# Performance work log

Hardware: AMD Instinct MI355X
Metric: run time of the kernel (lower is better)

## Reference

```python
import jax, jax.numpy as jnp
import numpy as np

NUM_NET = 2
V = 100000
D = 128
B = 4096
K = 5
NS = 10
HYP1 = 0.1
HYP2 = 0.1
HYP3 = 0.1


def setup_inputs() -> dict:
    key = jax.random.key(0)
    ks = jax.random.split(key, 10)
    ri = lambda k, shape: jax.random.randint(k, shape, 0, V, dtype=jnp.int32)
    return {
        "node_tables": jax.random.normal(ks[0], (NUM_NET, V, D), jnp.float32) * 0.1,
        "neigh_tables": jax.random.normal(ks[1], (NUM_NET, V, D), jnp.float32) * 0.1,
        "nodes_idx": ri(ks[2], (NUM_NET, B)),
        "neigh_idx": ri(ks[3], (NUM_NET, B, K)),
        "role_idx": ri(ks[4], (NUM_NET, NUM_NET, B)),
        "neg_main": ri(ks[5], (NUM_NET, B, K * NS)),
        "neg_node": ri(ks[6], (NUM_NET, NUM_NET, B, 1 * NS)),
        "neg_cross": ri(ks[7], (NUM_NET, NUM_NET, B, K * NS)),
        "neg_role": ri(ks[8], (NUM_NET, NUM_NET, B, 1 * NS)),
    }


def _pos_loss(ctx, node):
    # ctx: (B, M, D), node: (B, D) -> mean over all logsigmoid(ctx . node)
    return jax.nn.log_sigmoid(jnp.einsum("bmd,bd->bm", ctx, node)).mean()


def _neg_loss(neg_ctx, node):
    # ctx embeddings are negated: logsigmoid(-(neg . node)), sum over samples, mean over batch
    return jax.nn.log_sigmoid(-jnp.einsum("bmd,bd->bm", neg_ctx, node)).sum(axis=1).mean()


def reference(node_tables, neigh_tables, nodes_idx, neigh_idx, role_idx,
              neg_main, neg_node, neg_cross, neg_role):
    cost = []
    for i in range(NUM_NET):
        node_emb = node_tables[i][nodes_idx[i]]          # (B, D)
        # main SGNS loss on view i (neigh tables)
        neigh_emb = neigh_tables[i][neigh_idx[i]]        # (B, K, D)
        c = _pos_loss(neigh_emb, node_emb) + _neg_loss(neigh_tables[i][neg_main[i]], node_emb)
        cost.append(c)
        # cross-view node alignment (node tables of j at same node indices)
        for j in range(NUM_NET):
            if j != i:
                ctx = node_tables[j][nodes_idx[i]][:, None, :]   # (B, 1, D)
                c = _pos_loss(ctx, node_emb) + _neg_loss(node_tables[j][neg_node[i, j]], node_emb)
                cost.append(HYP1 * c)
        # cross-view neighbor loss (neigh tables of j at view-i neighbor indices)
        for j in range(NUM_NET):
            if j != i:
                ctx = neigh_tables[j][neigh_idx[i]]              # (B, K, D)
                c = _pos_loss(ctx, node_emb) + _neg_loss(neigh_tables[j][neg_cross[i, j]], node_emb)
                cost.append(HYP2 * c)
        # role-based loss (node tables of all j at role indices)
        for j in range(NUM_NET):
            ctx = node_tables[j][role_idx[i, j]][:, None, :]     # (B, 1, D)
            c = _pos_loss(ctx, node_emb) + _neg_loss(node_tables[j][neg_role[i, j]], node_emb)
            cost.append(HYP3 * c)
    total = cost[0]
    for c in cost[1:]:
        total = total + c
    return -total / len(cost)
```

## Files before the change

kernel.cpp:

```cpp
#include <hip/hip_runtime.h>

#define NUM_NET 2
#define V 100000
#define D 128
#define B 4096
#define K 5
#define NS 10

#define W_A (1.0f/20480.0f)
#define W_B (1.0f/4096.0f)
#define W_C (0.1f/4096.0f)
#define W_D (0.1f/20480.0f)

#define NBINS 64
#define PIPE 4

template <int CTRL>
__device__ __forceinline__ float dpp_xadd(float v) {
    int r = __builtin_amdgcn_update_dpp(0, __float_as_int(v), CTRL, 0xF, 0xF, true);
    return v + __int_as_float(r);
}

__device__ __forceinline__ float lsig(float x) {
    return fminf(x, 0.0f) - __logf(1.0f + __expf(-fabsf(x)));
}

__global__ __launch_bounds__(256) void rmne_main(
    const float* __restrict__ node_tables,
    const float* __restrict__ neigh_tables,
    const int*   __restrict__ nodes_idx,
    const int*   __restrict__ neigh_idx,
    const int*   __restrict__ role_idx,
    const int*   __restrict__ neg_main,
    const int*   __restrict__ neg_node,
    const int*   __restrict__ neg_cross,
    const int*   __restrict__ neg_role,
    float*       __restrict__ ws)
{
    const int tid  = threadIdx.x;
    const int lane = tid & 63;
    const int wave = tid >> 6;
    const int unit = blockIdx.x * 4 + wave;
    const int i = unit >> 12;
    const int b = unit & (B - 1);
    const int j = 1 - i;

    int pk[3];
    #pragma unroll
    for (int s = 0; s < 3; ++s) {
        int d = lane + 64 * s;
        int idx = 0; int tab = 0;
        if      (d <   5) { idx = neigh_idx[(i*B + b)*K + d];             tab = 2 + i; }
        else if (d <  55) { idx = neg_main[(i*B + b)*50 + (d-5)];         tab = 2 + i; }
        else if (d <  56) { idx = nodes_idx[i*B + b];                     tab = j;     }
        else if (d <  66) { idx = neg_node[((i*2+j)*B + b)*NS + (d-56)];  tab = j;     }
        else if (d <  71) { idx = neigh_idx[(i*B + b)*K + (d-66)];        tab = 2 + j; }
        else if (d < 121) { idx = neg_cross[((i*2+j)*B + b)*50 + (d-71)]; tab = 2 + j; }
        else if (d < 122) { idx = role_idx[(i*2+0)*B + b];                tab = 0;     }
        else if (d < 132) { idx = neg_role[((i*2+0)*B + b)*NS + (d-122)]; tab = 0;     }
        else if (d < 133) { idx = role_idx[(i*2+1)*B + b];                tab = 1;     }
        else if (d < 143) { idx = neg_role[((i*2+1)*B + b)*NS + (d-133)]; tab = 1;     }
        pk[s] = idx | (tab << 20);
    }

    const int l16     = lane & 15;
    const int quarter = lane >> 4;
    const int nrow    = nodes_idx[i*B + b];
    const float4* nep = (const float4*)(node_tables + ((size_t)i*V + (size_t)nrow)*D) + l16*2;
    const float4 ne0 = nep[0];
    const float4 ne1 = nep[1];

    float4 c0b[PIPE], c1b[PIPE];

    auto issue = [&](int t) {
        int s   = t >> 4;
        int src = (4*t + quarter) & 63;
        int p   = __shfl(pk[s], src, 64);
        int idx = p & 0xFFFFF;
        int tab = p >> 20;
        const float* base = (tab & 2) ? neigh_tables : node_tables;
        const float4* row = (const float4*)(base + ((size_t)(tab & 1)*V + (size_t)idx)*D) + l16*2;
        c0b[t & (PIPE-1)] = row[0];
        c1b[t & (PIPE-1)] = row[1];
    };

    float accA = 0.0f, accB = 0.0f, accC = 0.0f, accG = 0.0f;

    #pragma unroll
    for (int t = 0; t < PIPE; ++t) issue(t);

    #pragma unroll
    for (int t = 0; t < 36; ++t) {
        if (t + PIPE < 36) issue(t + PIPE);
        float4 c0 = c0b[t & (PIPE-1)];
        float4 c1 = c1b[t & (PIPE-1)];
        float pp = ne0.x*c0.x + ne0.y*c0.y + ne0.z*c0.z + ne0.w*c0.w
                 + ne1.x*c1.x + ne1.y*c1.y + ne1.z*c1.z + ne1.w*c1.w;
        pp = dpp_xadd<0xB1>(pp);
        pp = dpp_xadd<0x4E>(pp);
        pp = dpp_xadd<0x124>(pp);
        pp = dpp_xadd<0x128>(pp);

        if (t == 0) {
            accA += lsig(pp);
        } else if (t == 1) {
            float x  = (quarter == 0) ? pp : -pp;
            float mw = (quarter == 0) ? W_A : W_B;
            accG = fmaf(mw, lsig(x), accG);
        } else if (t <= 12) {
            accB += lsig(-pp);
        } else if (t == 13) {
            float x  = (quarter == 3) ? pp : -pp;
            float mw = (quarter == 3) ? W_C : W_B;
            accG = fmaf(mw, lsig(x), accG);
        } else if (t <= 15) {
            accC += lsig(-pp);
        } else if (t == 16) {
            float x  = (quarter >= 2) ? pp : -pp;
            float mw = (quarter >= 2) ? W_D : W_C;
            accG = fmaf(mw, lsig(x), accG);
        } else if (t == 17) {
            float x  = (quarter == 3) ? -pp : pp;
            float mw = (quarter == 3) ? W_C : W_D;
            accG = fmaf(mw, lsig(x), accG);
        } else if (t <= 29) {
            accC += lsig(-pp);
        } else if (t == 30) {
            float x = (quarter == 1) ? pp : -pp;
            accC += lsig(x);
        } else if (t <= 32) {
            accC += lsig(-pp);
        } else if (t == 33) {
            float x = (quarter == 0) ? pp : -pp;
            accC += lsig(x);
        } else if (t == 34) {
            accC += lsig(-pp);
        } else {
            float ls = lsig(-pp);
            accC += (quarter == 3) ? 0.0f : ls;
        }
    }

    float acc = W_A*accA + W_B*accB + W_C*accC + accG;

    acc += __shfl_xor(acc, 16, 64);
    acc += __shfl_xor(acc, 32, 64);

    __shared__ float wsum[4];
    if (lane == 0) wsum[wave] = acc;
    __syncthreads();
    if (tid == 0) {
        float s = wsum[0] + wsum[1] + wsum[2] + wsum[3];
        atomicAdd(ws + (blockIdx.x & (NBINS - 1)), s);
    }
}

__global__ void rmne_finalize(const float* __restrict__ ws, float* __restrict__ out)
{
    float v = ws[threadIdx.x];
    v += __shfl_xor(v, 1, 64);
    v += __shfl_xor(v, 2, 64);
    v += __shfl_xor(v, 4, 64);
    v += __shfl_xor(v, 8, 64);
    v += __shfl_xor(v, 16, 64);
    v += __shfl_xor(v, 32, 64);
    if (threadIdx.x == 0) out[0] = v * (-1.0f / 10.0f);
}

extern "C" void kernel_launch(void* const* d_in, const int* in_sizes, int n_in,
                              void* d_out, int out_size, void* d_ws, size_t ws_size,
                              hipStream_t stream) {
    const float* node_tables  = (const float*)d_in[0];
    const float* neigh_tables = (const float*)d_in[1];
    const int*   nodes_idx    = (const int*)d_in[2];
    const int*   neigh_idx    = (const int*)d_in[3];
    const int*   role_idx     = (const int*)d_in[4];
    const int*   neg_main     = (const int*)d_in[5];
    const int*   neg_node     = (const int*)d_in[6];
    const int*   neg_cross    = (const int*)d_in[7];
    const int*   neg_role     = (const int*)d_in[8];
    float* ws  = (float*)d_ws;
    float* out = (float*)d_out;

    hipMemsetAsync(ws, 0, NBINS * sizeof(float), stream);
    rmne_main<<<2048, 256, 0, stream>>>(node_tables, neigh_tables, nodes_idx, neigh_idx,
                                        role_idx, neg_main, neg_node, neg_cross, neg_role, ws);
    rmne_finalize<<<1, 64, 0, stream>>>(ws, out);
}
```

Measured before the change: 255.4 us.

## Hand-schedule gather loads with inline asm and explicit vmcnt waits

Row gathers now go through inline global_load_dwordx4 pairs, and each step waits only on the oldest outstanding load with an exact s_waitcnt vmcnt count, so several row fetches stay in flight. The loop is fully compile-time unrolled so the buffer slots and branch selection are constants, and each refill is issued after that step's compute. Each lane now reads two 16-byte chunks 256 bytes apart instead of 32 contiguous bytes, so 16 lanes cover a contiguous 256-byte span per instruction. Inline asm and sched barriers limit the compiler's own scheduling, and the hand-written wait counts must match the issue order exactly.

```diff
diff --git a/kernel.cpp b/kernel.cpp
--- a/kernel.cpp
+++ b/kernel.cpp
@@ -1,4 +1,5 @@
 #include <hip/hip_runtime.h>
+#include <utility>
 
 #define NUM_NET 2
 #define V 100000
@@ -13,7 +14,16 @@
 #define W_D (0.1f/20480.0f)
 
 #define NBINS 64
-#define PIPE 4
+#define DEPTH 4
+
+template <class F, int... Is>
+__device__ __forceinline__ void sfor_impl(F&& f, std::integer_sequence<int, Is...>) {
+    (f(std::integral_constant<int, Is>{}), ...);
+}
+template <int N, class F>
+__device__ __forceinline__ void sfor(F&& f) {
+    sfor_impl((F&&)f, std::make_integer_sequence<int, N>{});
+}
 
 template <int CTRL>
 __device__ __forceinline__ float dpp_xadd(float v) {
@@ -23,6 +33,20 @@
 
 __device__ __forceinline__ float lsig(float x) {
     return fminf(x, 0.0f) - __logf(1.0f + __expf(-fabsf(x)));
+}
+
+__device__ __forceinline__ void gload2(float4& d0, float4& d1, const float* addr) {
+    asm volatile("global_load_dwordx4 %0, %2, off\n\t"
+                 "global_load_dwordx4 %1, %2, off offset:256"
+                 : "=&v"(d0), "=&v"(d1)
+                 : "v"(addr)
+                 : "memory");
+}
+
+template <int N>
+__device__ __forceinline__ void waitfor() {
+    asm volatile("s_waitcnt vmcnt(%0)" :: "i"(N) : "memory");
+    __builtin_amdgcn_sched_barrier(0);
 }
 
 __global__ __launch_bounds__(256) void rmne_main(
@@ -66,34 +90,37 @@
     const int l16     = lane & 15;
     const int quarter = lane >> 4;
     const int nrow    = nodes_idx[i*B + b];
-    const float4* nep = (const float4*)(node_tables + ((size_t)i*V + (size_t)nrow)*D) + l16*2;
-    const float4 ne0 = nep[0];
-    const float4 ne1 = nep[1];
-
-    float4 c0b[PIPE], c1b[PIPE];
-
-    auto issue = [&](int t) {
-        int s   = t >> 4;
-        int src = (4*t + quarter) & 63;
-        int p   = __shfl(pk[s], src, 64);
+    const float* nep  = node_tables + ((size_t)i*V + (size_t)nrow)*D + l16*4;
+
+    float4 c0b[DEPTH], c1b[DEPTH];
+    float4 ne0, ne1;
+
+    auto issue = [&](auto tc) {
+        constexpr int T = decltype(tc)::value;
+        constexpr int S = T >> 4;
+        int src = (4*T + quarter) & 63;
+        int p   = __shfl(pk[S], src, 64);
         int idx = p & 0xFFFFF;
         int tab = p >> 20;
         const float* base = (tab & 2) ? neigh_tables : node_tables;
-        const float4* row = (const float4*)(base + ((size_t)(tab & 1)*V + (size_t)idx)*D) + l16*2;
-        c0b[t & (PIPE-1)] = row[0];
-        c1b[t & (PIPE-1)] = row[1];
+        const float* addr = base + ((size_t)(tab & 1)*V + (size_t)idx)*D + l16*4;
+        gload2(c0b[T & (DEPTH-1)], c1b[T & (DEPTH-1)], addr);
     };
 
+    asm volatile("s_waitcnt vmcnt(0)" ::: "memory");
+
+    gload2(ne0, ne1, nep);
+    sfor<DEPTH>([&](auto tc) { issue(tc); });
+
     float accA = 0.0f, accB = 0.0f, accC = 0.0f, accG = 0.0f;
 
-    #pragma unroll
-    for (int t = 0; t < PIPE; ++t) issue(t);
-
-    #pragma unroll
-    for (int t = 0; t < 36; ++t) {
-        if (t + PIPE < 36) issue(t + PIPE);
-        float4 c0 = c0b[t & (PIPE-1)];
-        float4 c1 = c1b[t & (PIPE-1)];
+    sfor<36>([&](auto tc) {
+        constexpr int T   = decltype(tc)::value;
+        constexpr int INF = (36 - T) < DEPTH ? (36 - T) : DEPTH;
+        waitfor<2*(INF-1)>();
+
+        float4 c0 = c0b[T & (DEPTH-1)];
+        float4 c1 = c1b[T & (DEPTH-1)];
         float pp = ne0.x*c0.x + ne0.y*c0.y + ne0.z*c0.z + ne0.w*c0.w
                  + ne1.x*c1.x + ne1.y*c1.y + ne1.z*c1.z + ne1.w*c1.w;
         pp = dpp_xadd<0xB1>(pp);
@@ -101,45 +128,47 @@
         pp = dpp_xadd<0x124>(pp);
         pp = dpp_xadd<0x128>(pp);
 
-        if (t == 0) {
+        if constexpr (T == 0) {
             accA += lsig(pp);
-        } else if (t == 1) {
+        } else if constexpr (T == 1) {
             float x  = (quarter == 0) ? pp : -pp;
             float mw = (quarter == 0) ? W_A : W_B;
             accG = fmaf(mw, lsig(x), accG);
-        } else if (t <= 12) {
+        } else if constexpr (T <= 12) {
             accB += lsig(-pp);
-        } else if (t == 13) {
+        } else if constexpr (T == 13) {
             float x  = (quarter == 3) ? pp : -pp;
             float mw = (quarter == 3) ? W_C : W_B;
             accG = fmaf(mw, lsig(x), accG);
-        } else if (t <= 15) {
-            accC += lsig(-pp);
-        } else if (t == 16) {
+        } else if constexpr (T <= 15) {
+            accC += lsig(-pp);
+        } else if constexpr (T == 16) {
             float x  = (quarter >= 2) ? pp : -pp;
             float mw = (quarter >= 2) ? W_D : W_C;
             accG = fmaf(mw, lsig(x), accG);
-        } else if (t == 17) {
+        } else if constexpr (T == 17) {
             float x  = (quarter == 3) ? -pp : pp;
             float mw = (quarter == 3) ? W_C : W_D;
             accG = fmaf(mw, lsig(x), accG);
-        } else if (t <= 29) {
-            accC += lsig(-pp);
-        } else if (t == 30) {
+        } else if constexpr (T <= 29) {
+            accC += lsig(-pp);
+        } else if constexpr (T == 30) {
             float x = (quarter == 1) ? pp : -pp;
             accC += lsig(x);
-        } else if (t <= 32) {
-            accC += lsig(-pp);
-        } else if (t == 33) {
+        } else if constexpr (T <= 32) {
+            accC += lsig(-pp);
+        } else if constexpr (T == 33) {
             float x = (quarter == 0) ? pp : -pp;
             accC += lsig(x);
-        } else if (t == 34) {
+        } else if constexpr (T == 34) {
             accC += lsig(-pp);
         } else {
             float ls = lsig(-pp);
             accC += (quarter == 3) ? 0.0f : ls;
         }
-    }
+
+        if constexpr (T + DEPTH < 36) issue(std::integral_constant<int, T + DEPTH>{});
+    });
 
     float acc = W_A*accA + W_B*accB + W_C*accC + accG;
 
```

New measurement: 263.2 us. 1.03x slower.
